# Kernel optimization log

Hardware: AMD Instinct MI355X
Metric: run time of the kernel (lower is better)

## Reference

```python
import jax, jax.numpy as jnp
import numpy as np

QA = 4  # quaternion dimension (qa in the torch code)


def _bingham_sample(lam, key):
    """ACG rejection sampler for Bingham(lam), lam > 0, shape [N, 4].
    Faithful to bingham_rj: resample rejected rows until all accepted.
    Implemented with a fixed-shape lax.while_loop (resample everything,
    keep accepted rows via where) so it is jit-compatible."""
    sigacginv = 1.0 + 2.0 * lam            # [N,4]
    sig = jnp.sqrt(1.0 / sigacginv)        # SigACG, per-component std
    N = lam.shape[0]
    X0 = jnp.zeros((N, QA), lam.dtype)
    acc0 = jnp.zeros((N,), dtype=bool)

    half_qa = QA / 2.0
    log_qa = jnp.log(jnp.asarray(QA, lam.dtype))

    def cond(state):
        _, acc, _ = state
        return ~jnp.all(acc)

    def body(state):
        X, acc, key = state
        key, k1, k2 = jax.random.split(key, 3)
        yp = jax.random.normal(k1, (N, QA), lam.dtype) * sig
        y = yp / jnp.linalg.norm(yp, axis=1, keepdims=True)
        y2 = y * y
        lratio = (-jnp.sum(y2 * lam, axis=1)
                  - half_qa * log_qa
                  + 0.5 * (QA - 1)
                  + half_qa * jnp.log(jnp.sum(y2 * sigacginv, axis=1)))
        u = jax.random.uniform(k2, (N,), lam.dtype)
        # torch code: X[indx] = y (overwrite not-yet-accepted), then decide accept
        X = jnp.where(acc[:, None], X, y)
        acc = acc | (jnp.log(u) < lratio)
        return X, acc, key

    X, _, _ = jax.lax.while_loop(cond, body, (X0, acc0, key))
    return X


def _make_E(qn):
    """Build z_Q [N,4,4] from unit quaternions, exactly as reparameterize_rj."""
    q0, q1, q2, q3 = qn[:, 0], qn[:, 1], qn[:, 2], qn[:, 3]
    r1 = jnp.stack([q0, -q1, -q2, q3], axis=-1)
    r2 = jnp.stack([q1, q0, q3, q2], axis=-1)
    r3 = jnp.stack([q2, -q3, q0, -q1], axis=-1)
    r4 = jnp.stack([q3, q2, -q1, -q0], axis=-1)
    return jnp.stack([r1, r2, r3, r4], axis=1)  # rows stacked along dim 1


def setup_inputs() -> dict:
    key = jax.random.key(0)
    kq, kz = jax.random.split(key)
    N = 1048576
    q = jax.random.normal(kq, (N, 4), jnp.float32)
    # strictly negative, monotonically decreasing concentrations (Z0<Z1<Z2 in |.|)
    dZ = jax.random.uniform(kz, (N, 3), jnp.float32, minval=1e-3, maxval=100.0)
    Zbatch = -jnp.cumsum(dZ, axis=1)  # [N,3], all < 0
    return {"q": q, "Zbatch": Zbatch, "seed": 42}


def reference(q, Zbatch, seed):
    # F.normalize on the quaternion output (done in forward before reparameterize_rj)
    qn = q / jnp.linalg.norm(q, axis=1, keepdims=True)
    E = _make_E(qn)                                              # [N,4,4]
    N = q.shape[0]
    Zexp = jnp.concatenate(
        [jnp.full((N, 1), -1e-6, Zbatch.dtype), Zbatch], axis=1)  # [N,4], all < 0
    lam = -Zexp                                                   # lam > 0
    X = _bingham_sample(lam, jax.random.key(seed))                # [N,4]
    # torch.bmm(E.transpose(1,2), X.unsqueeze(2)).squeeze() == E^T @ x per row
    return jnp.einsum('nij,ni->nj', E, X)
```

## Files before the change

### kernel.cpp

```cpp
#include <hip/hip_runtime.h>
#include <cstdint>


#define DEVI __device__ __forceinline__
#define MAXT 96
#define GRID 512
#define NT 256
#define CMAX 2048
#define GANGA 56
#define NG 16
#define GW 4

DEVI uint32_t rotl32(uint32_t v, int s) { return (v << s) | (v >> (32 - s)); }

DEVI void tf2x32(uint32_t k0, uint32_t k1, uint32_t x0, uint32_t x1,
                 uint32_t& o0, uint32_t& o1) {
  const uint32_t kx = k0 ^ k1 ^ 0x1BD11BDAu;
  x0 += k0; x1 += k1;
#define TFR(r) x0 += x1; x1 = rotl32(x1, (r)); x1 ^= x0;
  TFR(13) TFR(15) TFR(26) TFR(6)
  x0 += k1; x1 += kx + 1u;
  TFR(17) TFR(29) TFR(16) TFR(24)
  x0 += kx; x1 += k0 + 2u;
  TFR(13) TFR(15) TFR(26) TFR(6)
  x0 += k0; x1 += k1 + 3u;
  TFR(17) TFR(29) TFR(16) TFR(24)
  x0 += k1; x1 += kx + 4u;
  TFR(13) TFR(15) TFR(26) TFR(6)
  x0 += kx; x1 += k0 + 5u;
#undef TFR
  o0 = x0; o1 = x1;
}

DEVI void tf_round5(uint32_t x0[5], uint32_t x1[5], int rr) {
#pragma unroll
  for (int j = 0; j < 5; ++j) {
    x0[j] += x1[j];
    x1[j] = rotl32(x1[j], rr);
    x1[j] ^= x0[j];
  }
}
DEVI void tf_inj5(uint32_t x0[5], uint32_t x1[5],
                  const uint32_t* sa, const uint32_t* sb, uint32_t add) {
#pragma unroll
  for (int j = 0; j < 5; ++j) { x0[j] += sa[j]; x1[j] += sb[j] + add; }
}

DEVI float u01_from_bits(uint32_t bits) {
  return __fsub_rn(__uint_as_float(0x3f800000u | (bits >> 9)), 1.0f);
}

DEVI void trial5(uint4 ck, uint32_t base, uint32_t ctr, float u[5]) {
  uint32_t s0[5], s1[5], s2k[5], x0[5], x1[5];
#pragma unroll
  for (int j = 0; j < 5; ++j) {
    uint32_t k0 = (j < 4) ? ck.x : ck.z;
    uint32_t k1 = (j < 4) ? ck.y : ck.w;
    s0[j] = k0; s1[j] = k1; s2k[j] = k0 ^ k1 ^ 0x1BD11BDAu;
    uint32_t c = (j < 4) ? (base + (uint32_t)j) : ctr;
    x0[j] = k0;
    x1[j] = c + k1;
  }
  tf_round5(x0, x1, 13); tf_round5(x0, x1, 15);
  tf_round5(x0, x1, 26); tf_round5(x0, x1, 6);
  tf_inj5(x0, x1, s1, s2k, 1u);
  tf_round5(x0, x1, 17); tf_round5(x0, x1, 29);
  tf_round5(x0, x1, 16); tf_round5(x0, x1, 24);
  tf_inj5(x0, x1, s2k, s0, 2u);
  tf_round5(x0, x1, 13); tf_round5(x0, x1, 15);
  tf_round5(x0, x1, 26); tf_round5(x0, x1, 6);
  tf_inj5(x0, x1, s0, s1, 3u);
  tf_round5(x0, x1, 17); tf_round5(x0, x1, 29);
  tf_round5(x0, x1, 16); tf_round5(x0, x1, 24);
  tf_inj5(x0, x1, s1, s2k, 4u);
  tf_round5(x0, x1, 13); tf_round5(x0, x1, 15);
  tf_round5(x0, x1, 26); tf_round5(x0, x1, 6);
  tf_inj5(x0, x1, s2k, s0, 5u);
#pragma unroll
  for (int j = 0; j < 5; ++j) u[j] = u01_from_bits(x0[j] ^ x1[j]);
}

template <int K>
DEVI void xla_logf_pos_k(const float* xf, float* out) {
  float e[K], m[K], z[K], y[K];
#pragma unroll
  for (int j = 0; j < K; ++j) {
    uint32_t bits = __float_as_uint(xf[j]);
    e[j] = (float)((int)(bits >> 23) - 126);
    m[j] = __uint_as_float((bits & 0x007fffffu) | 0x3f000000u);
    bool mc = m[j] < 0.70710678118654752440f;
    float e_lo = __fsub_rn(e[j], 1.0f);
    float m_lo = __fadd_rn(__fsub_rn(m[j], 1.0f), m[j]);
    float m_hi = __fsub_rn(m[j], 1.0f);
    e[j] = mc ? e_lo : e[j];
    m[j] = mc ? m_lo : m_hi;
    z[j] = __fmul_rn(m[j], m[j]);
    y[j] = 7.0376836292e-2f;
  }
  const float LC[8] = {-1.1514610310e-1f,  1.1676998740e-1f,
                       -1.2420140846e-1f,  1.4249322787e-1f,
                       -1.6668057665e-1f,  2.0000714765e-1f,
                       -2.4999993993e-1f,  3.3333331174e-1f};
#pragma unroll
  for (int s = 0; s < 8; ++s)
#pragma unroll
    for (int j = 0; j < K; ++j)
      y[j] = __fadd_rn(__fmul_rn(y[j], m[j]), LC[s]);
#pragma unroll
  for (int j = 0; j < K; ++j) {
    float t = __fmul_rn(__fmul_rn(y[j], m[j]), z[j]);
    t = __fadd_rn(t, __fmul_rn(e[j], -2.12194440e-4f));
    t = __fsub_rn(t, __fmul_rn(z[j], 0.5f));
    float r = __fadd_rn(m[j], t);
    out[j] = __fadd_rn(r, __fmul_rn(e[j], 0.693359375f));
  }
}

DEVI void xla_erfinv4_logu(const float* xin, float uu, float* res,
                           float& lg_uu) {
  float v[4], vp1[5], big[5], w[4], q[4], p[4];
  bool c[4];
#pragma unroll
  for (int j = 0; j < 4; ++j) {
    v[j] = -__fmul_rn(xin[j], xin[j]);
    vp1[j] = __fadd_rn(v[j], 1.0f);
  }
  vp1[4] = uu;
  xla_logf_pos_k<5>(vp1, big);
  lg_uu = big[4];
#pragma unroll
  for (int j = 0; j < 4; ++j) {
    float small = __fmul_rn(__fadd_rn(__fmul_rn(-0.5f, v[j]), 1.0f), v[j]);
    float l1p = (fabsf(v[j]) < 1e-4f) ? small : big[j];
    w[j] = -l1p;
    c[j] = (w[j] < 5.0f);
    float qc = __fsub_rn(w[j], 2.5f);
    float qr = __fsub_rn(sqrtf(w[j]), 3.0f);
    q[j] = c[j] ? qc : qr;
    p[j] = c[j] ? 2.81022636e-08f : -0.000200214257f;
  }
  const float CF[8] = { 3.43273939e-07f, -3.5233877e-06f, -4.39150654e-06f,
                        0.00021858087f,  -0.00125372503f, -0.00417768164f,
                        0.246640727f,     1.50140941f};
  const float CR[8] = { 0.000100950558f,  0.00134934322f, -0.00367342844f,
                        0.00573950773f,  -0.0076224613f,   0.00943887047f,
                        1.00167406f,      2.83297682f};
#pragma unroll
  for (int s = 0; s < 8; ++s)
#pragma unroll
    for (int j = 0; j < 4; ++j)
      p[j] = __fadd_rn(__fmul_rn(p[j], q[j]), c[j] ? CF[s] : CR[s]);
#pragma unroll
  for (int j = 0; j < 4; ++j) res[j] = __fmul_rn(p[j], xin[j]);
}

DEVI bool trial_eval(uint4 ck, int r,
                     float lam1, float lam2, float lam3,
                     float sgi1, float sgi2, float sgi3,
                     float sig1, float sig2, float sig3,
                     float sgi0, float sig0,
                     float& ry0, float& ry1, float& ry2, float& ry3) {
  const uint32_t base = ((uint32_t)r) * 4u;

  float u5[5];
  trial5(ck, base, (uint32_t)r, u5);
  float uu = u5[4];

  float xin[4];
#pragma unroll
  for (int j = 0; j < 4; ++j) {
    float x = __fadd_rn(__fmul_rn(u5[j], 2.0f), -0.99999994f);
    xin[j] = fmaxf(-0.99999994f, x);
  }
  float er[4], lg_uu;
  xla_erfinv4_logu(xin, uu, er, lg_uu);

  float y0 = __fmul_rn(__fmul_rn(1.41421356237309504880f, er[0]), sig0);
  float y1 = __fmul_rn(__fmul_rn(1.41421356237309504880f, er[1]), sig1);
  float y2v = __fmul_rn(__fmul_rn(1.41421356237309504880f, er[2]), sig2);
  float y3 = __fmul_rn(__fmul_rn(1.41421356237309504880f, er[3]), sig3);

  float n2 = __fmul_rn(y0, y0);
  n2 = __fadd_rn(n2, __fmul_rn(y1, y1));
  n2 = __fadd_rn(n2, __fmul_rn(y2v, y2v));
  n2 = __fadd_rn(n2, __fmul_rn(y3, y3));
  float nr = sqrtf(n2);
  y0 = __fdiv_rn(y0, nr); y1 = __fdiv_rn(y1, nr);
  y2v = __fdiv_rn(y2v, nr); y3 = __fdiv_rn(y3, nr);

  float s0q = __fmul_rn(y0, y0), s1q = __fmul_rn(y1, y1);
  float s2q = __fmul_rn(y2v, y2v), s3q = __fmul_rn(y3, y3);

  float s1v = __fmul_rn(s0q, 1e-6f);
  s1v = __fadd_rn(s1v, __fmul_rn(s1q, lam1));
  s1v = __fadd_rn(s1v, __fmul_rn(s2q, lam2));
  s1v = __fadd_rn(s1v, __fmul_rn(s3q, lam3));

  float s2v = __fmul_rn(s0q, sgi0);
  s2v = __fadd_rn(s2v, __fmul_rn(s1q, sgi1));
  s2v = __fadd_rn(s2v, __fmul_rn(s2q, sgi2));
  s2v = __fadd_rn(s2v, __fmul_rn(s3q, sgi3));

  float lg_s2[1];
  xla_logf_pos_k<1>(&s2v, lg_s2);

  float lr = __fsub_rn(-s1v, 2.7725887298583984f);
  lr = __fadd_rn(lr, 1.5f);
  lr = __fadd_rn(lr, __fmul_rn(2.0f, lg_s2[0]));

  float lu = (uu > 0.0f) ? lg_uu : -__builtin_inff();

  ry0 = y0; ry1 = y1; ry2 = y2v; ry3 = y3;
  return (lu < lr);
}

__global__ __launch_bounds__(256, 2) void campose_kernel(
    const float* __restrict__ q, const float* __restrict__ Z,
    float* __restrict__ out, const int* __restrict__ seedp, int N, int C) {
  __shared__ uint4 chain[MAXT + 1];
  __shared__ float4 rc4a[CMAX];
  __shared__ float4 rc4b[CMAX];
  __shared__ float rc1[CMAX];
  __shared__ uint32_t next_row;
  __shared__ uint32_t wm;

  const int tid = threadIdx.x;
  const int lane = tid & 63;
  const int rbeg = blockIdx.x * C;
  const int rend = min(N, rbeg + C);
  const int crows = rend - rbeg;
  if (tid == 0) { next_row = (uint32_t)(rbeg + 192); wm = 0u; }

  for (int i = tid; i < crows; i += NT) {
    float z0 = Z[(size_t)(rbeg + i) * 3 + 0];
    float z1 = Z[(size_t)(rbeg + i) * 3 + 1];
    float z2 = Z[(size_t)(rbeg + i) * 3 + 2];
    float l1 = -z0, l2 = -z1, l3 = -z2;
    float g1 = __fadd_rn(1.0f, __fmul_rn(2.0f, l1));
    float g2 = __fadd_rn(1.0f, __fmul_rn(2.0f, l2));
    float g3 = __fadd_rn(1.0f, __fmul_rn(2.0f, l3));
    float s1_ = sqrtf(__fdiv_rn(1.0f, g1));
    float s2_ = sqrtf(__fdiv_rn(1.0f, g2));
    float s3_ = sqrtf(__fdiv_rn(1.0f, g3));
    rc4a[i] = make_float4(g1, g2, g3, s1_);
    rc4b[i] = make_float4(s2_, s3_, l1, l2);
    rc1[i] = l3;
  }
  __syncthreads();

  const int wave = tid >> 6;
  if (wave == 0) {
    uint32_t ka = 0u, kb = (uint32_t)seedp[0];
    uint32_t x1i = (lane == 2) ? 0u : (uint32_t)(lane + 1);
    for (int t = 0; t < MAXT; ++t) {
      uint32_t o0 = 0u, o1 = 0u;
      if (lane < 3) tf2x32(ka, kb, 0u, x1i, o0, o1);
      uint32_t s1a = __shfl(o0, 0, 64), s1b = __shfl(o1, 0, 64);
      uint32_t s2a = __shfl(o0, 1, 64), s2b = __shfl(o1, 1, 64);
      if (lane == 0) chain[t] = make_uint4(s1a, s1b, s2a, s2b);
      ka = __shfl(o0, 2, 64); kb = __shfl(o1, 2, 64);
      __threadfence_block();
      if (lane == 0) *(volatile uint32_t*)&wm = (uint32_t)(t + 1);
    }
    if (lane == 0) chain[MAXT] = make_uint4(0u, 0u, 0u, 0u);
    __threadfence_block();
    if (lane == 0) *(volatile uint32_t*)&wm = (uint32_t)(MAXT + 1);
  }

  const float sgi0 = __fadd_rn(1.0f, __fmul_rn(2.0f, 1e-6f));
  const float sig0 = sqrtf(__fdiv_rn(1.0f, sgi0));

  int r, rn;
  if (wave == 0) {
    r  = (int)atomicAdd(&next_row, 1u);
    rn = (int)atomicAdd(&next_row, 1u);
  } else {
    r  = rbeg + (tid - 64);
    rn = (int)atomicAdd(&next_row, 1u);
  }
  bool have = (r < rend);
  float lam1 = 0, lam2 = 0, lam3 = 0;
  float sgi1 = 1, sgi2 = 1, sgi3 = 1;
  float sig1 = 1, sig2 = 1, sig3 = 1;
  if (have) {
    int li = r - rbeg;
    float4 A = rc4a[li], B = rc4b[li];
    sgi1 = A.x; sgi2 = A.y; sgi3 = A.z; sig1 = A.w;
    sig2 = B.x; sig3 = B.y; lam1 = B.z; lam2 = B.w;
    lam3 = rc1[li];
  }

  uint32_t wml = *(volatile uint32_t*)&wm;
  while (wml < 1u) wml = *(volatile uint32_t*)&wm;
  __threadfence_block();
  const uint4 ck0 = chain[0];
  uint4 ck = ck0;
  int t = 0;

  while (true) {
    uint64_t msk = __ballot(have);
    if (__popcll(msk) <= GANGA) break;
    if (have) {
      if (wml < (uint32_t)(t + 2)) {
        uint32_t w_ = *(volatile uint32_t*)&wm;
        while (w_ < (uint32_t)(t + 2)) w_ = *(volatile uint32_t*)&wm;
        __threadfence_block();
        wml = w_;
      }
      uint4 ckn = chain[t + 1];

      float y0, y1, y2v, y3;
      bool alr = trial_eval(ck, r, lam1, lam2, lam3, sgi1, sgi2, sgi3,
                            sig1, sig2, sig3, sgi0, sig0, y0, y1, y2v, y3);

      ++t;
      if (alr || (t >= MAXT)) {
        *reinterpret_cast<float4*>(out + (size_t)r * 4) =
            make_float4(y0, y1, y2v, y3);
        r = rn;
        int li = (r < rend ? r : rend - 1) - rbeg;
        float4 A = rc4a[li], B = rc4b[li];
        sgi1 = A.x; sgi2 = A.y; sgi3 = A.z; sig1 = A.w;
        sig2 = B.x; sig3 = B.y; lam1 = B.z; lam2 = B.w;
        lam3 = rc1[li];
        t = 0;
        ck = ck0;
        have = (r < rend);
        rn = (int)atomicAdd(&next_row, 1u);
      } else {
        ck = ckn;
      }
    }
  }

  uint64_t mask = __ballot(have);
  if (mask) {
    if (wml < (uint32_t)(MAXT + 1)) {
      uint32_t w_ = *(volatile uint32_t*)&wm;
      while (w_ < (uint32_t)(MAXT + 1)) w_ = *(volatile uint32_t*)&wm;
      __threadfence_block();
      wml = w_;
    }
    while (mask) {
      int G = __popcll(mask); if (G > NG) G = NG;
      const int g = lane >> 2, k = lane & 3;
      const bool gact = (g < G);
      const int gidx = gact ? g : 0;
      uint64_t m = mask;
      int sl = __ffsll((unsigned long long)m) - 1;
#pragma unroll
      for (int i = 1; i < NG; ++i) {
        m &= m - 1;
        int b = __ffsll((unsigned long long)m) - 1;
        sl = (i <= gidx && b >= 0) ? b : sl;
      }
      int rg = __shfl(r, sl, 64);
      int tg = __shfl(t, sl, 64);
      int li = rg - rbeg;
      float4 A = rc4a[li], B = rc4b[li];
      float G1 = A.x, G2 = A.y, G3 = A.z, S1 = A.w;
      float S2 = B.x, S3 = B.y, L1 = B.z, L2 = B.w;
      float L3 = rc1[li];
      int ts = tg + k;
      int tsc = ts < (MAXT - 1) ? ts : (MAXT - 1);
      uint4 cks = chain[tsc];
      float y0, y1, y2v, y3;
      bool alr = trial_eval(cks, rg, L1, L2, L3, G1, G2, G3,
                            S1, S2, S3, sgi0, sig0, y0, y1, y2v, y3);
      bool acc = alr || (ts >= MAXT - 1);
      uint64_t bal = __ballot(acc && gact);
      uint64_t gb = (bal >> (g * GW)) & 0xfull;
      int kwin = gb ? (__ffsll((unsigned long long)gb) - 1) : GW;
      if (gact && k == kwin) {
        *reinterpret_cast<float4*>(out + (size_t)rg * 4) =
            make_float4(y0, y1, y2v, y3);
      }
      int myidx = __popcll(mask & ((1ull << lane) - 1ull));
      if (have && myidx < G) {
        uint64_t gbb = (bal >> (myidx * GW)) & 0xfull;
        if (gbb) {
          r = rn;
          t = 0;
          have = (r < rend);
          rn = (int)atomicAdd(&next_row, 1u);
        } else {
          t += GW;
        }
      }
      mask = __ballot(have);
    }
  }

  __syncthreads();
  for (int i = rbeg + tid; i < rend; i += NT) {
    float4 yv = *reinterpret_cast<const float4*>(out + (size_t)i * 4);
    float4 qv = *reinterpret_cast<const float4*>(q + (size_t)i * 4);
    float a = qv.x, b = qv.y, c = qv.z, d = qv.w;
    float qn2 = __fmul_rn(a, a);
    qn2 = __fadd_rn(qn2, __fmul_rn(b, b));
    qn2 = __fadd_rn(qn2, __fmul_rn(c, c));
    qn2 = __fadd_rn(qn2, __fmul_rn(d, d));
    float qnr = sqrtf(qn2);
    a = __fdiv_rn(a, qnr); b = __fdiv_rn(b, qnr);
    c = __fdiv_rn(c, qnr); d = __fdiv_rn(d, qnr);
    float y0 = yv.x, y1 = yv.y, y2v = yv.z, y3 = yv.w;
    float o0v = __fadd_rn(__fadd_rn(__fadd_rn(__fmul_rn(a, y0), __fmul_rn(b, y1)),
                                    __fmul_rn(c, y2v)), __fmul_rn(d, y3));
    float o1v = __fadd_rn(__fadd_rn(__fadd_rn(__fmul_rn(-b, y0), __fmul_rn(a, y1)),
                                    __fmul_rn(-d, y2v)), __fmul_rn(c, y3));
    float o2v = __fadd_rn(__fadd_rn(__fadd_rn(__fmul_rn(-c, y0), __fmul_rn(d, y1)),
                                    __fmul_rn(a, y2v)), __fmul_rn(-b, y3));
    float o3v = __fadd_rn(__fadd_rn(__fadd_rn(__fmul_rn(d, y0), __fmul_rn(c, y1)),
                                    __fmul_rn(-b, y2v)), __fmul_rn(-a, y3));
    *reinterpret_cast<float4*>(out + (size_t)i * 4) =
        make_float4(o0v, o1v, o2v, o3v);
  }
}

extern "C" void kernel_launch(void* const* d_in, const int* in_sizes, int n_in,
                              void* d_out, int out_size, void* d_ws, size_t ws_size,
                              hipStream_t stream) {
  const float* q = (const float*)d_in[0];
  const float* Z = (const float*)d_in[1];
  const int* seed = (const int*)d_in[2];
  float* out = (float*)d_out;
  int N = in_sizes[0] / 4;

  int nb = GRID;
  int C = (N + nb - 1) / nb;
  if (C > CMAX) {
    nb = (N + CMAX - 1) / CMAX;
    C = (N + nb - 1) / nb;
  }
  campose_kernel<<<nb, NT, 0, stream>>>(q, Z, out, seed, N, C);
}
```

Measured before the change: 156.2 us.

## Fuse quaternion rotation into per-row store and add uniform erfinv fast path

```diff
diff --git a/kernel.cpp b/kernel.cpp
--- a/kernel.cpp
+++ b/kernel.cpp
@@ -118,7 +118,7 @@
 
 DEVI void xla_erfinv4_logu(const float* xin, float uu, float* res,
                            float& lg_uu) {
-  float v[4], vp1[5], big[5], w[4], q[4], p[4];
+  float v[4], vp1[5], big[5], w[4];
   bool c[4];
 #pragma unroll
   for (int j = 0; j < 4; ++j) {
@@ -134,10 +134,6 @@
     float l1p = (fabsf(v[j]) < 1e-4f) ? small : big[j];
     w[j] = -l1p;
     c[j] = (w[j] < 5.0f);
-    float qc = __fsub_rn(w[j], 2.5f);
-    float qr = __fsub_rn(sqrtf(w[j]), 3.0f);
-    q[j] = c[j] ? qc : qr;
-    p[j] = c[j] ? 2.81022636e-08f : -0.000200214257f;
   }
   const float CF[8] = { 3.43273939e-07f, -3.5233877e-06f, -4.39150654e-06f,
                         0.00021858087f,  -0.00125372503f, -0.00417768164f,
@@ -145,13 +141,38 @@
   const float CR[8] = { 0.000100950558f,  0.00134934322f, -0.00367342844f,
                         0.00573950773f,  -0.0076224613f,   0.00943887047f,
                         1.00167406f,      2.83297682f};
-#pragma unroll
-  for (int s = 0; s < 8; ++s)
-#pragma unroll
-    for (int j = 0; j < 4; ++j)
-      p[j] = __fadd_rn(__fmul_rn(p[j], q[j]), c[j] ? CF[s] : CR[s]);
-#pragma unroll
-  for (int j = 0; j < 4; ++j) res[j] = __fmul_rn(p[j], xin[j]);
+  bool slow = !(c[0] && c[1] && c[2] && c[3]);
+  if (__ballot(slow) == 0ull) {
+    float q[4], p[4];
+#pragma unroll
+    for (int j = 0; j < 4; ++j) {
+      q[j] = __fsub_rn(w[j], 2.5f);
+      p[j] = 2.81022636e-08f;
+    }
+#pragma unroll
+    for (int s = 0; s < 8; ++s)
+#pragma unroll
+      for (int j = 0; j < 4; ++j)
+        p[j] = __fadd_rn(__fmul_rn(p[j], q[j]), CF[s]);
+#pragma unroll
+    for (int j = 0; j < 4; ++j) res[j] = __fmul_rn(p[j], xin[j]);
+  } else {
+    float q[4], p[4];
+#pragma unroll
+    for (int j = 0; j < 4; ++j) {
+      float qc = __fsub_rn(w[j], 2.5f);
+      float qr = __fsub_rn(sqrtf(w[j]), 3.0f);
+      q[j] = c[j] ? qc : qr;
+      p[j] = c[j] ? 2.81022636e-08f : -0.000200214257f;
+    }
+#pragma unroll
+    for (int s = 0; s < 8; ++s)
+#pragma unroll
+      for (int j = 0; j < 4; ++j)
+        p[j] = __fadd_rn(__fmul_rn(p[j], q[j]), c[j] ? CF[s] : CR[s]);
+#pragma unroll
+    for (int j = 0; j < 4; ++j) res[j] = __fmul_rn(p[j], xin[j]);
+  }
 }
 
 DEVI bool trial_eval(uint4 ck, int r,
@@ -212,6 +233,29 @@
 
   ry0 = y0; ry1 = y1; ry2 = y2v; ry3 = y3;
   return (lu < lr);
+}
+
+DEVI void store_final(float* __restrict__ out, int r,
+                      float qa, float qb, float qc_, float qd,
+                      float y0, float y1, float y2v, float y3) {
+  float a = qa, b = qb, c = qc_, d = qd;
+  float qn2 = __fmul_rn(a, a);
+  qn2 = __fadd_rn(qn2, __fmul_rn(b, b));
+  qn2 = __fadd_rn(qn2, __fmul_rn(c, c));
+  qn2 = __fadd_rn(qn2, __fmul_rn(d, d));
+  float qnr = sqrtf(qn2);
+  a = __fdiv_rn(a, qnr); b = __fdiv_rn(b, qnr);
+  c = __fdiv_rn(c, qnr); d = __fdiv_rn(d, qnr);
+  float o0v = __fadd_rn(__fadd_rn(__fadd_rn(__fmul_rn(a, y0), __fmul_rn(b, y1)),
+                                  __fmul_rn(c, y2v)), __fmul_rn(d, y3));
+  float o1v = __fadd_rn(__fadd_rn(__fadd_rn(__fmul_rn(-b, y0), __fmul_rn(a, y1)),
+                                  __fmul_rn(-d, y2v)), __fmul_rn(c, y3));
+  float o2v = __fadd_rn(__fadd_rn(__fadd_rn(__fmul_rn(-c, y0), __fmul_rn(d, y1)),
+                                  __fmul_rn(a, y2v)), __fmul_rn(-b, y3));
+  float o3v = __fadd_rn(__fadd_rn(__fadd_rn(__fmul_rn(d, y0), __fmul_rn(c, y1)),
+                                  __fmul_rn(-b, y2v)), __fmul_rn(-a, y3));
+  *reinterpret_cast<float4*>(out + (size_t)r * 4) =
+      make_float4(o0v, o1v, o2v, o3v);
 }
 
 __global__ __launch_bounds__(256, 2) void campose_kernel(
@@ -282,12 +326,20 @@
   float lam1 = 0, lam2 = 0, lam3 = 0;
   float sgi1 = 1, sgi2 = 1, sgi3 = 1;
   float sig1 = 1, sig2 = 1, sig3 = 1;
+  float cq0 = 0, cq1 = 0, cq2 = 0, cq3 = 0;
+  float nq0 = 0, nq1 = 0, nq2 = 0, nq3 = 0;
   if (have) {
     int li = r - rbeg;
     float4 A = rc4a[li], B = rc4b[li];
     sgi1 = A.x; sgi2 = A.y; sgi3 = A.z; sig1 = A.w;
     sig2 = B.x; sig3 = B.y; lam1 = B.z; lam2 = B.w;
     lam3 = rc1[li];
+    float4 qv = *reinterpret_cast<const float4*>(q + (size_t)r * 4);
+    cq0 = qv.x; cq1 = qv.y; cq2 = qv.z; cq3 = qv.w;
+  }
+  if (rn < rend) {
+    float4 qv = *reinterpret_cast<const float4*>(q + (size_t)rn * 4);
+    nq0 = qv.x; nq1 = qv.y; nq2 = qv.z; nq3 = qv.w;
   }
 
   uint32_t wml = *(volatile uint32_t*)&wm;
@@ -315,9 +367,9 @@
 
       ++t;
       if (alr || (t >= MAXT)) {
-        *reinterpret_cast<float4*>(out + (size_t)r * 4) =
-            make_float4(y0, y1, y2v, y3);
+        store_final(out, r, cq0, cq1, cq2, cq3, y0, y1, y2v, y3);
         r = rn;
+        cq0 = nq0; cq1 = nq1; cq2 = nq2; cq3 = nq3;
         int li = (r < rend ? r : rend - 1) - rbeg;
         float4 A = rc4a[li], B = rc4b[li];
         sgi1 = A.x; sgi2 = A.y; sgi3 = A.z; sig1 = A.w;
@@ -327,6 +379,10 @@
         ck = ck0;
         have = (r < rend);
         rn = (int)atomicAdd(&next_row, 1u);
+        if (rn < rend) {
+          float4 qv = *reinterpret_cast<const float4*>(q + (size_t)rn * 4);
+          nq0 = qv.x; nq1 = qv.y; nq2 = qv.z; nq3 = qv.w;
+        }
       } else {
         ck = ckn;
       }
@@ -372,8 +428,8 @@
       uint64_t gb = (bal >> (g * GW)) & 0xfull;
       int kwin = gb ? (__ffsll((unsigned long long)gb) - 1) : GW;
       if (gact && k == kwin) {
-        *reinterpret_cast<float4*>(out + (size_t)rg * 4) =
-            make_float4(y0, y1, y2v, y3);
+        float4 qv = *reinterpret_cast<const float4*>(q + (size_t)rg * 4);
+        store_final(out, rg, qv.x, qv.y, qv.z, qv.w, y0, y1, y2v, y3);
       }
       int myidx = __popcll(mask & ((1ull << lane) - 1ull));
       if (have && myidx < G) {
@@ -390,31 +446,6 @@
       mask = __ballot(have);
     }
   }
-
-  __syncthreads();
-  for (int i = rbeg + tid; i < rend; i += NT) {
-    float4 yv = *reinterpret_cast<const float4*>(out + (size_t)i * 4);
-    float4 qv = *reinterpret_cast<const float4*>(q + (size_t)i * 4);
-    float a = qv.x, b = qv.y, c = qv.z, d = qv.w;
-    float qn2 = __fmul_rn(a, a);
-    qn2 = __fadd_rn(qn2, __fmul_rn(b, b));
-    qn2 = __fadd_rn(qn2, __fmul_rn(c, c));
-    qn2 = __fadd_rn(qn2, __fmul_rn(d, d));
-    float qnr = sqrtf(qn2);
-    a = __fdiv_rn(a, qnr); b = __fdiv_rn(b, qnr);
-    c = __fdiv_rn(c, qnr); d = __fdiv_rn(d, qnr);
-    float y0 = yv.x, y1 = yv.y, y2v = yv.z, y3 = yv.w;
-    float o0v = __fadd_rn(__fadd_rn(__fadd_rn(__fmul_rn(a, y0), __fmul_rn(b, y1)),
-                                    __fmul_rn(c, y2v)), __fmul_rn(d, y3));
-    float o1v = __fadd_rn(__fadd_rn(__fadd_rn(__fmul_rn(-b, y0), __fmul_rn(a, y1)),
-                                    __fmul_rn(-d, y2v)), __fmul_rn(c, y3));
-    float o2v = __fadd_rn(__fadd_rn(__fadd_rn(__fmul_rn(-c, y0), __fmul_rn(d, y1)),
-                                    __fmul_rn(a, y2v)), __fmul_rn(-b, y3));
-    float o3v = __fadd_rn(__fadd_rn(__fadd_rn(__fmul_rn(d, y0), __fmul_rn(c, y1)),
-                                    __fmul_rn(-b, y2v)), __fmul_rn(-a, y3));
-    *reinterpret_cast<float4*>(out + (size_t)i * 4) =
-        make_float4(o0v, o1v, o2v, o3v);
-  }
 }
 
 extern "C" void kernel_launch(void* const* d_in, const int* in_sizes, int n_in,
```

New measurement: 159.5 us. +2.1%, slower.
